# Optimization experiments

Measured on AMD Instinct MI355X. Metric: run time of the kernel, lower is better.

## Reference

```python
import jax, jax.numpy as jnp
import numpy as np

EPS = 1e-5

def conv1d(x, w, b, pad):
    # x: [B,C_in,S], w: [C_out,C_in,K] -> [B,C_out,S]
    y = jax.lax.conv_general_dilated(x, w, window_strides=(1,), padding=[(pad, pad)],
                                     dimension_numbers=('NCH', 'OIH', 'NCH'))
    return y + b[None, :, None]

def bn(x, gamma, beta, mean, var):
    # inference-mode BatchNorm1d over channel dim of [B,C,S]
    scale = gamma * jax.lax.rsqrt(var + EPS)
    shift = beta - mean * scale
    return x * scale[None, :, None] + shift[None, :, None]

def setup_inputs() -> dict:
    key = jax.random.key(0)
    ks = jax.random.split(key, 16)
    B, S, D, C, K = 32, 2048, 128, 256, 5
    x = jax.random.normal(ks[0], (B, S, D), dtype=jnp.float32)
    start_padding_indices = jax.random.randint(ks[1], (B,), 0, S, dtype=jnp.int64 if jax.config.jax_enable_x64 else jnp.int32)
    def conv_init(k, co, ci, kk):
        fan = ci * kk
        return jax.random.normal(k, (co, ci, kk), dtype=jnp.float32) / np.sqrt(fan)
    W1 = conv_init(ks[2], C, D, K); b1 = jnp.zeros((C,), jnp.float32)
    g1 = jnp.ones((C,), jnp.float32); be1 = jnp.zeros((C,), jnp.float32)
    m1 = jax.random.normal(ks[3], (C,), dtype=jnp.float32) * 0.1
    v1 = jax.random.uniform(ks[4], (C,), dtype=jnp.float32, minval=0.5, maxval=1.5)
    W2 = conv_init(ks[5], C, C, K); b2 = jnp.zeros((C,), jnp.float32)
    g2 = jnp.ones((C,), jnp.float32); be2 = jnp.zeros((C,), jnp.float32)
    m2 = jax.random.normal(ks[6], (C,), dtype=jnp.float32) * 0.1
    v2 = jax.random.uniform(ks[7], (C,), dtype=jnp.float32, minval=0.5, maxval=1.5)
    Wf = conv_init(ks[8], D, C, 1); bf = jnp.zeros((D,), jnp.float32)
    return {"x": x, "start_padding_indices": start_padding_indices,
            "W1": W1, "b1": b1, "g1": g1, "be1": be1, "m1": m1, "v1": v1,
            "W2": W2, "b2": b2, "g2": g2, "be2": be2, "m2": m2, "v2": v2,
            "Wf": Wf, "bf": bf}

def reference(x, start_padding_indices, W1, b1, g1, be1, m1, v1,
              W2, b2, g2, be2, m2, v2, Wf, bf):
    B, S, D = x.shape
    K = W1.shape[-1]
    h = jnp.transpose(x, (0, 2, 1))                      # [B,D,S]
    h = jax.nn.relu(bn(conv1d(h, W1, b1, K // 2), g1, be1, m1, v1))
    h = jax.nn.relu(bn(conv1d(h, W2, b2, K // 2), g2, be2, m2, v2))
    h = conv1d(h, Wf, bf, 0)                             # [B,D,S]
    conv_out = jnp.transpose(h, (0, 2, 1))               # [B,S,D]
    # vectorized masked mean: -1 sentinel -> full length; 0 -> zeros
    lengths = jnp.where(start_padding_indices == -1, S, start_padding_indices)  # [B]
    mask = jnp.arange(S)[None, :] < lengths[:, None]     # [B,S]
    sums = jnp.sum(conv_out * mask[:, :, None].astype(conv_out.dtype), axis=1)  # [B,D]
    denom = jnp.maximum(lengths, 1).astype(conv_out.dtype)[:, None]
    pooled = jnp.where(lengths[:, None] > 0, sums / denom, jnp.zeros_like(sums))
    return pooled
```

## Files before the change

### kernel.cpp

```cpp
#include <hip/hip_runtime.h>

#define S_LEN 2048
#define NBATCH 32

typedef __bf16 bf16x8 __attribute__((ext_vector_type(8)));
typedef float f32x4 __attribute__((ext_vector_type(4)));
typedef unsigned short bf_t;

__device__ __forceinline__ unsigned short f2bf(float f) {
  __bf16 h = (__bf16)f;
  return __builtin_bit_cast(unsigned short, h);
}

#if __has_builtin(__builtin_amdgcn_global_load_lds)
#define USE_GLL 1
#else
#define USE_GLL 0
#endif

__device__ __forceinline__ void load_lds16(const void* g, void* ldsbase) {
#if USE_GLL
  __builtin_amdgcn_global_load_lds(
      (const __attribute__((address_space(1))) unsigned int*)g,
      (__attribute__((address_space(3))) unsigned int*)ldsbase, 16, 0, 0);
#else
  *(int4*)((char*)ldsbase + (threadIdx.x & 63) * 16) =
      *(const int4*)((const char*)g);
#endif
}

#define WAITV8  asm volatile("s_waitcnt vmcnt(8)" ::: "memory")
#define WAITV4  asm volatile("s_waitcnt vmcnt(4)" ::: "memory")
#define WAITV0  asm volatile("s_waitcnt vmcnt(0)" ::: "memory")

__global__ void convert_x(const float* __restrict__ x, bf_t* __restrict__ xb) {
  const size_t i = (size_t)blockIdx.x * blockDim.x + threadIdx.x;
  const float4 a = ((const float4*)x)[2 * i];
  const float4 c = ((const float4*)x)[2 * i + 1];
  ushort4 o0; o0.x = f2bf(a.x); o0.y = f2bf(a.y); o0.z = f2bf(a.z); o0.w = f2bf(a.w);
  ushort4 o1; o1.x = f2bf(c.x); o1.y = f2bf(c.y); o1.z = f2bf(c.z); o1.w = f2bf(c.w);
  ((ushort4*)xb)[2 * i] = o0;
  ((ushort4*)xb)[2 * i + 1] = o1;
}

__global__ void fold_bn(const float* __restrict__ b1, const float* __restrict__ g1,
                        const float* __restrict__ be1, const float* __restrict__ m1,
                        const float* __restrict__ v1,
                        const float* __restrict__ b2, const float* __restrict__ g2,
                        const float* __restrict__ be2, const float* __restrict__ m2,
                        const float* __restrict__ v2, float* __restrict__ abuf,
                        float* __restrict__ zp) {
  int c = threadIdx.x;
  if (c < 64) zp[c] = 0.f;
  if (c < 256) {
    float a1 = g1[c] * rsqrtf(v1[c] + 1e-5f);
    abuf[c] = a1;
    abuf[256 + c] = (b1[c] - m1[c]) * a1 + be1[c];
    float a2 = g2[c] * rsqrtf(v2[c] + 1e-5f);
    abuf[512 + c] = a2;
    abuf[768 + c] = (b2[c] - m2[c]) * a2 + be2[c];
  }
}

template <int CIN, int TAPS>
__global__ void prep_w2(const float* __restrict__ w, bf_t* __restrict__ wfm) {
  const int idx = blockIdx.x * 256 + threadIdx.x;
  constexpr int total = 256 * CIN * TAPS;
  if (idx >= total) return;
  const int j = idx & 7;
  const int l = (idx >> 3) & 63;
  const int f = (idx >> 9) & 7;
  const int wr = (idx >> 12) & 1;
  const int tg = idx >> 13;
  const int co = wr * 128 + f * 16 + (l & 15);
  const int cc = tg / (TAPS * 4);
  const int k = (tg / 4) % TAPS;
  const int q = tg & 3;
  const int ci = cc * 128 + q * 32 + (l >> 4) * 8 + j;
  wfm[idx] = f2bf(w[((size_t)co * CIN + ci) * TAPS + k]);
}

template <int CIN, int COUT, int TAPS>
__global__ void prep_w(const float* __restrict__ w, bf_t* __restrict__ wfm) {
  constexpr int T = CIN * TAPS / 32;
  const int idx = blockIdx.x * 256 + threadIdx.x;
  constexpr int total = COUT * CIN * TAPS;
  if (idx >= total) return;
  const int j = idx & 7;
  const int l = (idx >> 3) & 63;
  const int f = (idx >> 9) & 3;
  const int gt = idx >> 11;
  const int t = gt % T;
  const int g = gt / T;
  const int co = g * 64 + f * 16 + (l & 15);
  const int cc = t / (TAPS * 4);
  const int k = (t / 4) % TAPS;
  const int q = t & 3;
  const int ci = cc * 128 + q * 32 + (l >> 4) * 8 + j;
  wfm[idx] = f2bf(w[((size_t)co * CIN + ci) * TAPS + k]);
}

template <int CIN, int TAPS>
__device__ __forceinline__ void conv_body(
    const bf_t* __restrict__ xin, const bf_t* __restrict__ wfm,
    const float* __restrict__ alpha, const float* __restrict__ bias,
    const float* __restrict__ zp, bf_t* __restrict__ hout) {
  constexpr int HALO = (TAPS - 1) / 2;
  constexpr int P = (CIN / 128) * TAPS * 4;
  constexpr int NKT = P / 2;

  __shared__ char smem[131072];

  const int tid = threadIdx.x;
  const int l = tid & 63;
  const int wv = tid >> 6;
  const int wr = wv >> 2;
  const int wn = wv & 3;
  const int b = blockIdx.x >> 3;
  const int s0 = (blockIdx.x & 7) << 8;
  const int l15 = l & 15;
  const int l4 = l >> 4;
  const int wu16 = (tid - l) * 16;

  f32x4 acc[8][4] = {};

  auto STAGE_A = [&](int jt, int sub) {
    const char* src = (const char*)wfm + (size_t)(2 * jt + sub) * 16384;
    char* dst = smem + (jt & 1) * 32768 + sub * 16384;
    load_lds16(src + tid * 16, dst + wu16);
    load_lds16(src + 8192 + tid * 16, dst + 8192 + wu16);
  };

  auto STAGE_B = [&](int jt, int sub) {
    const int t = 2 * jt + sub;
    const int cc = t / (TAPS * 4);
    const int k = (t >> 2) % TAPS;
    const int q = t & 3;
    char* dst = smem + 65536 + (jt & 1) * 32768 + sub * 16384;
    const int r0 = tid >> 2;
    const int slot = ((r0 & 3) ^ ((r0 >> 2) & 3)) << 4;
    const char* srcb = (const char*)xin +
        ((size_t)b * S_LEN * CIN + cc * 128 + q * 32) * 2 +
        (((tid & 3) * 16) ^ slot);
    {
      const int s = s0 + r0 - HALO + k;
      const char* src = ((unsigned)s < (unsigned)S_LEN)
          ? srcb + (size_t)s * (CIN * 2) : ((const char*)zp + (((tid & 3) * 16) ^ slot));
      load_lds16(src, dst + wu16);
    }
    {
      const int s = s0 + r0 + 128 - HALO + k;
      const char* src = ((unsigned)s < (unsigned)S_LEN)
          ? srcb + (size_t)s * (CIN * 2) : ((const char*)zp + (((tid & 3) * 16) ^ slot));
      load_lds16(src, dst + 8192 + wu16);
    }
  };

  auto LDB = [&](const char* Bb, int sub, int r) -> bf16x8 {
    const int slot = (((r & 3) ^ ((r >> 2) & 3)) << 4);
    return *(const bf16x8*)(Bb + sub * 16384 + r * 64 + ((l4 * 16) ^ slot));
  };

  STAGE_A(0, 0); STAGE_A(0, 1); STAGE_B(0, 0); STAGE_B(0, 1);
  WAITV0;
  STAGE_A(1, 0); STAGE_B(1, 0);
  __builtin_amdgcn_s_barrier();

#pragma unroll 1
  for (int j = 0; j < NKT; ++j) {
    const char* Ab = smem + (j & 1) * 32768;
    const char* Bb = smem + 65536 + (j & 1) * 32768;

    {
      __builtin_amdgcn_s_setprio(1);
      bf16x8 afr[8], bfr[4];
#pragma unroll
      for (int f = 0; f < 8; ++f)
        afr[f] = *(const bf16x8*)(Ab + wr * 8192 + f * 1024 + l * 16);
#pragma unroll
      for (int n = 0; n < 4; ++n)
        bfr[n] = LDB(Bb, 0, wn * 64 + n * 16 + l15);
      if (j + 1 < NKT) { STAGE_B(j + 1, 1); STAGE_A(j + 1, 1); }
#pragma unroll
      for (int f = 0; f < 8; ++f)
#pragma unroll
        for (int n = 0; n < 4; ++n)
          acc[f][n] = __builtin_amdgcn_mfma_f32_16x16x32_bf16(
              afr[f], bfr[n], acc[f][n], 0, 0, 0);
      __builtin_amdgcn_s_setprio(0);
      if (j < NKT - 1) { WAITV8; } else { WAITV0; }
      __builtin_amdgcn_s_barrier();
      __builtin_amdgcn_sched_barrier(0);
    }

    {
      __builtin_amdgcn_s_setprio(1);
      bf16x8 afr[8], bfr[4];
#pragma unroll
      for (int f = 0; f < 8; ++f)
        afr[f] = *(const bf16x8*)(Ab + 16384 + wr * 8192 + f * 1024 + l * 16);
#pragma unroll
      for (int n = 0; n < 4; ++n)
        bfr[n] = LDB(Bb, 1, wn * 64 + n * 16 + l15);
      if (j + 2 < NKT) { STAGE_A(j + 2, 0); STAGE_B(j + 2, 0); }
#pragma unroll
      for (int f = 0; f < 8; ++f)
#pragma unroll
        for (int n = 0; n < 4; ++n)
          acc[f][n] = __builtin_amdgcn_mfma_f32_16x16x32_bf16(
              afr[f], bfr[n], acc[f][n], 0, 0, 0);
      __builtin_amdgcn_s_setprio(0);
      if (j <= NKT - 3) { WAITV8; } else if (j == NKT - 2) { WAITV4; }
      __builtin_amdgcn_s_barrier();
      __builtin_amdgcn_sched_barrier(0);
    }
  }

  WAITV0;
  __syncthreads();
  const int cobase = wr * 128;
#pragma unroll
  for (int f = 0; f < 8; ++f) {
    const int co0 = cobase + f * 16 + l4 * 4;
    const f32x4 al = *(const f32x4*)(alpha + co0);
    const f32x4 bi = *(const f32x4*)(bias + co0);
#pragma unroll
    for (int n = 0; n < 4; ++n) {
      const int sp = wn * 64 + n * 16 + l15;
      ushort4 pk;
      pk.x = f2bf(fmaxf(acc[f][n][0] * al[0] + bi[0], 0.f));
      pk.y = f2bf(fmaxf(acc[f][n][1] * al[1] + bi[1], 0.f));
      pk.z = f2bf(fmaxf(acc[f][n][2] * al[2] + bi[2], 0.f));
      pk.w = f2bf(fmaxf(acc[f][n][3] * al[3] + bi[3], 0.f));
      *(ushort4*)(smem + sp * 512 + ((co0 * 2) ^ ((sp & 7) << 4))) = pk;
    }
  }
  __syncthreads();
  {
    char* hb = (char*)hout + ((size_t)(b * S_LEN + s0) * 256) * 2;
#pragma unroll
    for (int k = 0; k < 16; ++k) {
      const int c = tid + k * 512;
      const int sp = c >> 5;
      const int col = (c & 31) * 16;
      const int4 v = *(const int4*)(smem + sp * 512 + (col ^ ((sp & 7) << 4)));
      *(int4*)(hb + (size_t)sp * 512 + col) = v;
    }
  }
}

__global__ __launch_bounds__(512, 2)
void conv_gemm_L1(const bf_t* __restrict__ xin, const bf_t* __restrict__ wfm,
                  const float* __restrict__ alpha, const float* __restrict__ bias,
                  const float* __restrict__ zp, bf_t* __restrict__ hout) {
  conv_body<128, 5>(xin, wfm, alpha, bias, zp, hout);
}

__global__ __launch_bounds__(512, 2)
void conv_gemm_L2(const bf_t* __restrict__ xin, const bf_t* __restrict__ wfm,
                  const float* __restrict__ alpha, const float* __restrict__ bias,
                  const float* __restrict__ zp, bf_t* __restrict__ hout) {
  conv_body<256, 5>(xin, wfm, alpha, bias, zp, hout);
}

__global__ __launch_bounds__(512, 4)
void conv_pool(const bf_t* __restrict__ xin, const bf_t* __restrict__ wfm,
               const float* __restrict__ bfin, const int* __restrict__ spi,
               float* __restrict__ gpart) {
  constexpr int CIN = 256;
  constexpr int T = 8;

  __shared__ char smem[128 * 256];
  __shared__ float red[4][128];

  const int tid = threadIdx.x;
  const int l = tid & 63;
  const int wv = tid >> 6;
  const int wr = wv >> 2;
  const int wn = wv & 3;
  const int nb = blockIdx.x;
  const int b = nb >> 4;
  const int st = nb & 15;
  const int s0 = st << 7;
  const int l15 = l & 15;
  const int l4 = l >> 4;

  f32x4 acc[4][2] = {};
  const bf_t* wbase = wfm + (size_t)wr * (T * 2048);

  for (int cc = 0; cc < 2; ++cc) {
    const char* src = (const char*)xin + ((size_t)b * S_LEN * CIN + cc * 128) * 2;
    for (int off = tid * 16; off < 128 * 256; off += 512 * 16) {
      const int row = off >> 8;
      const int c = off & 255;
      const int cs = c ^ ((row & 7) << 4);
      void* ldsbase = (void*)(smem + (off - l * 16));
      load_lds16(src + (size_t)(s0 + row) * (CIN * 2) + cs, ldsbase);
    }
    __syncthreads();

#pragma unroll
    for (int q = 0; q < 4; ++q) {
      const int t = cc * 4 + q;
      bf16x8 bfr[2];
#pragma unroll
      for (int fn = 0; fn < 2; ++fn) {
        const int row = wn * 32 + fn * 16 + l15;
        const int cb = q * 64 + l4 * 16;
        bfr[fn] = *(const bf16x8*)(smem + row * 256 + (cb ^ ((row & 7) << 4)));
      }
#pragma unroll
      for (int f = 0; f < 4; ++f) {
        const bf16x8 afr =
            *(const bf16x8*)(wbase + ((size_t)(t * 4 + f) * 64 + l) * 8);
        acc[f][0] = __builtin_amdgcn_mfma_f32_16x16x32_bf16(afr, bfr[0], acc[f][0], 0, 0, 0);
        acc[f][1] = __builtin_amdgcn_mfma_f32_16x16x32_bf16(afr, bfr[1], acc[f][1], 0, 0, 0);
      }
    }
    __syncthreads();
  }

  int len = spi[b];
  if (len < 0) len = S_LEN;

#pragma unroll
  for (int f = 0; f < 4; ++f) {
    const int co0 = wr * 64 + f * 16 + l4 * 4;
    const f32x4 bi = *(const f32x4*)(bfin + co0);
    f32x4 vs = {};
#pragma unroll
    for (int fn = 0; fn < 2; ++fn) {
      const int s = s0 + wn * 32 + fn * 16 + l15;
      const float m = (s < len) ? 1.f : 0.f;
      vs[0] += (acc[f][fn][0] + bi[0]) * m;
      vs[1] += (acc[f][fn][1] + bi[1]) * m;
      vs[2] += (acc[f][fn][2] + bi[2]) * m;
      vs[3] += (acc[f][fn][3] + bi[3]) * m;
    }
#pragma unroll
    for (int d = 1; d < 16; d <<= 1) {
      vs[0] += __shfl_xor(vs[0], d, 64);
      vs[1] += __shfl_xor(vs[1], d, 64);
      vs[2] += __shfl_xor(vs[2], d, 64);
      vs[3] += __shfl_xor(vs[3], d, 64);
    }
    if (l15 == 0) {
      red[wn][co0 + 0] = vs[0];
      red[wn][co0 + 1] = vs[1];
      red[wn][co0 + 2] = vs[2];
      red[wn][co0 + 3] = vs[3];
    }
  }
  __syncthreads();
  if (tid < 128) {
    float p = red[0][tid] + red[1][tid] + red[2][tid] + red[3][tid];
    gpart[((size_t)b * 16 + st) * 128 + tid] = p;
  }
}

__global__ void finalize(const float* __restrict__ gpart, const int* __restrict__ spi,
                         float* __restrict__ out) {
  const int b = blockIdx.x;
  const int d = threadIdx.x;
  float s = 0.f;
#pragma unroll
  for (int t = 0; t < 16; ++t) s += gpart[((size_t)b * 16 + t) * 128 + d];
  int len = spi[b];
  if (len < 0) len = S_LEN;
  float denom = (float)(len < 1 ? 1 : len);
  out[b * 128 + d] = s / denom;
}

extern "C" void kernel_launch(void* const* d_in, const int* in_sizes, int n_in,
                              void* d_out, int out_size, void* d_ws, size_t ws_size,
                              hipStream_t stream) {
  (void)in_sizes; (void)n_in; (void)out_size; (void)ws_size;
  const float* x = (const float*)d_in[0];
  const int* spi = (const int*)d_in[1];
  const float* W1 = (const float*)d_in[2];
  const float* b1 = (const float*)d_in[3];
  const float* g1 = (const float*)d_in[4];
  const float* be1 = (const float*)d_in[5];
  const float* m1 = (const float*)d_in[6];
  const float* v1 = (const float*)d_in[7];
  const float* W2 = (const float*)d_in[8];
  const float* b2 = (const float*)d_in[9];
  const float* g2 = (const float*)d_in[10];
  const float* be2 = (const float*)d_in[11];
  const float* m2 = (const float*)d_in[12];
  const float* v2 = (const float*)d_in[13];
  const float* Wf = (const float*)d_in[14];
  const float* bf_ = (const float*)d_in[15];
  float* out = (float*)d_out;

  char* ws = (char*)d_ws;
  float* zp   = (float*)(ws);
  bf_t* xb    = (bf_t*)(ws + 4096);
  bf_t* h1    = (bf_t*)(ws + 16781312);
  bf_t* h2    = (bf_t*)(ws + 50335744);
  bf_t* wf1   = (bf_t*)(ws + 83890176);
  bf_t* wf2   = (bf_t*)(ws + 84217856);
  bf_t* wff   = (bf_t*)(ws + 84873216);
  float* abuf = (float*)(ws + 84938752);
  float* gpart= (float*)(ws + 84942848);

  convert_x<<<4096, 256, 0, stream>>>(x, xb);
  fold_bn<<<1, 256, 0, stream>>>(b1, g1, be1, m1, v1, b2, g2, be2, m2, v2, abuf, zp);
  prep_w2<128, 5><<<640, 256, 0, stream>>>(W1, wf1);
  prep_w2<256, 5><<<1280, 256, 0, stream>>>(W2, wf2);
  prep_w<256, 128, 1><<<128, 256, 0, stream>>>(Wf, wff);

  conv_gemm_L1<<<256, 512, 0, stream>>>(xb, wf1, abuf, abuf + 256, zp, h1);
  conv_gemm_L2<<<256, 512, 0, stream>>>(h1, wf2, abuf + 512, abuf + 768, zp, h2);
  conv_pool<<<512, 512, 0, stream>>>(h2, wff, bf_, spi, gpart);
  finalize<<<32, 128, 0, stream>>>(gpart, spi, out);
}
```

Before: 104.6 us.

## Merge prep kernels into one launch and fuse finalize via last-block atomic

Combines the five preprocessing kernels (x conversion, BN folding, three weight repacks) into a single kernel that dispatches on block index. It also folds the finalize kernel into conv_pool: each block bumps an atomic counter after a threadfence, and the last block to arrive does the cross-tile reduction and division. This cuts the launch count from nine to four, removing launch gaps, in exchange for a serialized tail in one block and counter-reset logic.

```diff
diff --git a/kernel.cpp b/kernel.cpp
--- a/kernel.cpp
+++ b/kernel.cpp
@@ -33,71 +33,71 @@
 #define WAITV4  asm volatile("s_waitcnt vmcnt(4)" ::: "memory")
 #define WAITV0  asm volatile("s_waitcnt vmcnt(0)" ::: "memory")
 
-__global__ void convert_x(const float* __restrict__ x, bf_t* __restrict__ xb) {
-  const size_t i = (size_t)blockIdx.x * blockDim.x + threadIdx.x;
-  const float4 a = ((const float4*)x)[2 * i];
-  const float4 c = ((const float4*)x)[2 * i + 1];
-  ushort4 o0; o0.x = f2bf(a.x); o0.y = f2bf(a.y); o0.z = f2bf(a.z); o0.w = f2bf(a.w);
-  ushort4 o1; o1.x = f2bf(c.x); o1.y = f2bf(c.y); o1.z = f2bf(c.z); o1.w = f2bf(c.w);
-  ((ushort4*)xb)[2 * i] = o0;
-  ((ushort4*)xb)[2 * i + 1] = o1;
-}
-
-__global__ void fold_bn(const float* __restrict__ b1, const float* __restrict__ g1,
-                        const float* __restrict__ be1, const float* __restrict__ m1,
-                        const float* __restrict__ v1,
-                        const float* __restrict__ b2, const float* __restrict__ g2,
-                        const float* __restrict__ be2, const float* __restrict__ m2,
-                        const float* __restrict__ v2, float* __restrict__ abuf,
-                        float* __restrict__ zp) {
-  int c = threadIdx.x;
-  if (c < 64) zp[c] = 0.f;
-  if (c < 256) {
-    float a1 = g1[c] * rsqrtf(v1[c] + 1e-5f);
-    abuf[c] = a1;
-    abuf[256 + c] = (b1[c] - m1[c]) * a1 + be1[c];
-    float a2 = g2[c] * rsqrtf(v2[c] + 1e-5f);
-    abuf[512 + c] = a2;
-    abuf[768 + c] = (b2[c] - m2[c]) * a2 + be2[c];
-  }
-}
-
-template <int CIN, int TAPS>
-__global__ void prep_w2(const float* __restrict__ w, bf_t* __restrict__ wfm) {
-  const int idx = blockIdx.x * 256 + threadIdx.x;
-  constexpr int total = 256 * CIN * TAPS;
-  if (idx >= total) return;
-  const int j = idx & 7;
-  const int l = (idx >> 3) & 63;
-  const int f = (idx >> 9) & 7;
-  const int wr = (idx >> 12) & 1;
-  const int tg = idx >> 13;
-  const int co = wr * 128 + f * 16 + (l & 15);
-  const int cc = tg / (TAPS * 4);
-  const int k = (tg / 4) % TAPS;
-  const int q = tg & 3;
-  const int ci = cc * 128 + q * 32 + (l >> 4) * 8 + j;
-  wfm[idx] = f2bf(w[((size_t)co * CIN + ci) * TAPS + k]);
-}
-
-template <int CIN, int COUT, int TAPS>
-__global__ void prep_w(const float* __restrict__ w, bf_t* __restrict__ wfm) {
-  constexpr int T = CIN * TAPS / 32;
-  const int idx = blockIdx.x * 256 + threadIdx.x;
-  constexpr int total = COUT * CIN * TAPS;
-  if (idx >= total) return;
-  const int j = idx & 7;
-  const int l = (idx >> 3) & 63;
-  const int f = (idx >> 9) & 3;
-  const int gt = idx >> 11;
-  const int t = gt % T;
-  const int g = gt / T;
-  const int co = g * 64 + f * 16 + (l & 15);
-  const int cc = t / (TAPS * 4);
-  const int k = (t / 4) % TAPS;
-  const int q = t & 3;
-  const int ci = cc * 128 + q * 32 + (l >> 4) * 8 + j;
-  wfm[idx] = f2bf(w[((size_t)co * CIN + ci) * TAPS + k]);
+__global__ void prep_all(const float* __restrict__ x,
+                         const float* __restrict__ W1, const float* __restrict__ W2,
+                         const float* __restrict__ Wf,
+                         const float* __restrict__ b1, const float* __restrict__ g1,
+                         const float* __restrict__ be1, const float* __restrict__ m1,
+                         const float* __restrict__ v1,
+                         const float* __restrict__ b2, const float* __restrict__ g2,
+                         const float* __restrict__ be2, const float* __restrict__ m2,
+                         const float* __restrict__ v2,
+                         bf_t* __restrict__ xb, bf_t* __restrict__ wf1,
+                         bf_t* __restrict__ wf2, bf_t* __restrict__ wff,
+                         float* __restrict__ abuf, float* __restrict__ zp,
+                         unsigned int* __restrict__ cnt) {
+  const int bid = blockIdx.x;
+  if (bid < 4096) {
+    const size_t i = (size_t)bid * 256 + threadIdx.x;
+    const float4 a = ((const float4*)x)[2 * i];
+    const float4 c = ((const float4*)x)[2 * i + 1];
+    ushort4 o0; o0.x = f2bf(a.x); o0.y = f2bf(a.y); o0.z = f2bf(a.z); o0.w = f2bf(a.w);
+    ushort4 o1; o1.x = f2bf(c.x); o1.y = f2bf(c.y); o1.z = f2bf(c.z); o1.w = f2bf(c.w);
+    ((ushort4*)xb)[2 * i] = o0;
+    ((ushort4*)xb)[2 * i + 1] = o1;
+  } else if (bid < 6016) {
+    const float* w; bf_t* wfm; int idx; int CIN;
+    if (bid < 4736) { w = W1; wfm = wf1; idx = (bid - 4096) * 256 + threadIdx.x; CIN = 128; }
+    else            { w = W2; wfm = wf2; idx = (bid - 4736) * 256 + threadIdx.x; CIN = 256; }
+    const int TAPS = 5;
+    const int j = idx & 7;
+    const int l = (idx >> 3) & 63;
+    const int f = (idx >> 9) & 7;
+    const int wr = (idx >> 12) & 1;
+    const int tg = idx >> 13;
+    const int co = wr * 128 + f * 16 + (l & 15);
+    const int cc = tg / (TAPS * 4);
+    const int k = (tg / 4) % TAPS;
+    const int q = tg & 3;
+    const int ci = cc * 128 + q * 32 + (l >> 4) * 8 + j;
+    wfm[idx] = f2bf(w[((size_t)co * CIN + ci) * TAPS + k]);
+  } else if (bid < 6144) {
+    const int idx = (bid - 6016) * 256 + threadIdx.x;
+    const int T = 8;
+    const int j = idx & 7;
+    const int l = (idx >> 3) & 63;
+    const int f = (idx >> 9) & 3;
+    const int gt = idx >> 11;
+    const int t = gt % T;
+    const int g = gt / T;
+    const int co = g * 64 + f * 16 + (l & 15);
+    const int q = t & 3;
+    const int cc = t >> 2;
+    const int ci = cc * 128 + q * 32 + (l >> 4) * 8 + j;
+    wff[idx] = f2bf(Wf[(size_t)co * 256 + ci]);
+  } else {
+    int c = threadIdx.x;
+    if (c == 0) *cnt = 0;
+    if (c < 64) zp[c] = 0.f;
+    if (c < 256) {
+      float a1 = g1[c] * rsqrtf(v1[c] + 1e-5f);
+      abuf[c] = a1;
+      abuf[256 + c] = (b1[c] - m1[c]) * a1 + be1[c];
+      float a2 = g2[c] * rsqrtf(v2[c] + 1e-5f);
+      abuf[512 + c] = a2;
+      abuf[768 + c] = (b2[c] - m2[c]) * a2 + be2[c];
+    }
+  }
 }
 
 template <int CIN, int TAPS>
@@ -266,12 +266,14 @@
 __global__ __launch_bounds__(512, 4)
 void conv_pool(const bf_t* __restrict__ xin, const bf_t* __restrict__ wfm,
                const float* __restrict__ bfin, const int* __restrict__ spi,
-               float* __restrict__ gpart) {
+               float* __restrict__ gpart, unsigned int* __restrict__ cnt,
+               float* __restrict__ out) {
   constexpr int CIN = 256;
   constexpr int T = 8;
 
   __shared__ char smem[128 * 256];
   __shared__ float red[4][128];
+  __shared__ unsigned int sord;
 
   const int tid = threadIdx.x;
   const int l = tid & 63;
@@ -356,19 +358,25 @@
     float p = red[0][tid] + red[1][tid] + red[2][tid] + red[3][tid];
     gpart[((size_t)b * 16 + st) * 128 + tid] = p;
   }
-}
-
-__global__ void finalize(const float* __restrict__ gpart, const int* __restrict__ spi,
-                         float* __restrict__ out) {
-  const int b = blockIdx.x;
-  const int d = threadIdx.x;
-  float s = 0.f;
-#pragma unroll
-  for (int t = 0; t < 16; ++t) s += gpart[((size_t)b * 16 + t) * 128 + d];
-  int len = spi[b];
-  if (len < 0) len = S_LEN;
-  float denom = (float)(len < 1 ? 1 : len);
-  out[b * 128 + d] = s / denom;
+
+  __threadfence();
+  __syncthreads();
+  if (tid == 0) sord = atomicAdd(cnt, 1u);
+  __syncthreads();
+  if (sord == NBATCH * 16 - 1) {
+    __threadfence();
+    for (int i = tid; i < NBATCH * 128; i += 512) {
+      const int bb = i >> 7;
+      const int d = i & 127;
+      float s = 0.f;
+#pragma unroll
+      for (int t = 0; t < 16; ++t) s += gpart[((size_t)bb * 16 + t) * 128 + d];
+      int ln = spi[bb];
+      if (ln < 0) ln = S_LEN;
+      float denom = (float)(ln < 1 ? 1 : ln);
+      out[bb * 128 + d] = s / denom;
+    }
+  }
 }
 
 extern "C" void kernel_launch(void* const* d_in, const int* in_sizes, int n_in,
@@ -403,15 +411,13 @@
   bf_t* wff   = (bf_t*)(ws + 84873216);
   float* abuf = (float*)(ws + 84938752);
   float* gpart= (float*)(ws + 84942848);
-
-  convert_x<<<4096, 256, 0, stream>>>(x, xb);
-  fold_bn<<<1, 256, 0, stream>>>(b1, g1, be1, m1, v1, b2, g2, be2, m2, v2, abuf, zp);
-  prep_w2<128, 5><<<640, 256, 0, stream>>>(W1, wf1);
-  prep_w2<256, 5><<<1280, 256, 0, stream>>>(W2, wf2);
-  prep_w<256, 128, 1><<<128, 256, 0, stream>>>(Wf, wff);
-
+  unsigned int* cnt = (unsigned int*)(ws + 85204992);
+
+  prep_all<<<6145, 256, 0, stream>>>(x, W1, W2, Wf,
+                                     b1, g1, be1, m1, v1,
+                                     b2, g2, be2, m2, v2,
+                                     xb, wf1, wf2, wff, abuf, zp, cnt);
   conv_gemm_L1<<<256, 512, 0, stream>>>(xb, wf1, abuf, abuf + 256, zp, h1);
   conv_gemm_L2<<<256, 512, 0, stream>>>(h1, wf2, abuf + 512, abuf + 768, zp, h2);
-  conv_pool<<<512, 512, 0, stream>>>(h2, wff, bf_, spi, gpart);
-  finalize<<<32, 128, 0, stream>>>(gpart, spi, out);
-}
+  conv_pool<<<512, 512, 0, stream>>>(h2, wff, bf_, spi, gpart, cnt, out);
+}
```

New measurement: 159.7 us. +52.6%, slower.
